# Optimization experiments

Measured on AMD Instinct MI355X. Metric: run time of the kernel, lower is better.

## Reference

```python
import jax, jax.numpy as jnp
import numpy as np

EPS = 1e-9
KERNEL = 3


def kernel_tile(x, kernel, stride):
    """im2col-style patch extraction. x: [B,H,W,...] -> [B,OH,OW,kernel*kernel,depth]."""
    B, H, W = x.shape[:3]
    depth = int(np.prod(x.shape[3:]))
    x = x.reshape(B, H, W, depth)
    OH = (H - kernel) // stride + 1
    OW = (W - kernel) // stride + 1
    patches = jnp.stack(
        [x[:, i:i + (OH - 1) * stride + 1:stride, j:j + (OW - 1) * stride + 1:stride, :]
         for i in range(kernel) for j in range(kernel)], axis=3)
    return patches  # [B,OH,OW,k*k,depth]


def em_routing(votes, i_act, beta_v, beta_a, routings):
    # votes: [B,S,S,I,O,16], i_act: [B,S,S,I], beta_*: [1,1,1,O]
    I, O = votes.shape[-3], votes.shape[-2]
    rr = jnp.full((I, O, 1), 1.0 / O, dtype=votes.dtype)
    i_act = i_act[..., None, None]           # [B,S,S,I,1,1]
    bv = beta_v[..., None, :, None]          # [1,1,1,1,O,1]
    ba = beta_a[..., None, :, None]
    it_min, it_max = 1.0, min(float(routings), 3.0)
    o_mean = o_act = None
    for it in range(routings):
        inv_temp = it_min + (it_max - it_min) * it / max(1.0, routings - 1.0)
        # M-step
        rr_prime = rr * i_act                                        # [B,S,S,I,O,1]
        rr_sum = jnp.sum(rr_prime, axis=-3, keepdims=True)           # [B,S,S,1,O,1]
        o_mean = jnp.sum(rr_prime * votes, axis=-3, keepdims=True) / rr_sum  # [B,S,S,1,O,16]
        o_stdv = jnp.sqrt(jnp.sum(rr_prime * jnp.square(votes - o_mean), axis=-3, keepdims=True) / rr_sum)
        o_cost = (bv + jnp.log(o_stdv + EPS)) * rr_sum               # [B,S,S,1,O,16]
        o_act = jax.nn.sigmoid(inv_temp * (ba - jnp.sum(o_cost, axis=-1, keepdims=True)))  # [B,S,S,1,O,1]
        if it < routings - 1:
            # E-step: log Gaussian prob of each vote under each output capsule
            o_p = (-jnp.sum(jnp.square(votes - o_mean) / (2.0 * jnp.square(o_stdv)), axis=-1, keepdims=True)
                   - jnp.sum(jnp.log(o_stdv + EPS), axis=-1, keepdims=True))  # [B,S,S,I,O,1]
            zz = jnp.log(o_act + EPS) + o_p
            rr = jax.nn.softmax(zz, axis=-2)                          # softmax over O
    pose = jnp.squeeze(o_mean, axis=-3)      # [B,S,S,O,16]
    act = jnp.squeeze(o_act, axis=(-3, -1))  # [B,S,S,O]
    return pose, act


def setup_inputs() -> dict:
    key = jax.random.key(0)
    ks = jax.random.split(key, 5)
    B, H, W, I_SIZE, O_SIZE = 4, 14, 14, 32, 32
    inputs_pose = jax.random.normal(ks[0], (B, H, W, I_SIZE, 4, 4), dtype=jnp.float32)
    inputs_activation = jax.random.uniform(ks[1], (B, H, W, I_SIZE), dtype=jnp.float32)
    w = jax.random.normal(ks[2], (1, 3 * 3 * I_SIZE, O_SIZE, 4, 4), dtype=jnp.float32)
    beta_v = 0.1 * jax.random.normal(ks[3], (1, 1, 1, O_SIZE), dtype=jnp.float32)
    beta_a = 0.1 * jax.random.normal(ks[4], (1, 1, 1, O_SIZE), dtype=jnp.float32)
    return {"inputs_pose": inputs_pose, "inputs_activation": inputs_activation,
            "w": w, "beta_v": beta_v, "beta_a": beta_a, "stride": 1, "routings": 3}


def reference(inputs_pose, inputs_activation, w, beta_v, beta_a, stride, routings):
    B = inputs_pose.shape[0]
    pose_size = inputs_pose.shape[-1]            # 4
    i_size = inputs_pose.shape[3]
    o_size = w.shape[2]
    tp = kernel_tile(inputs_pose, KERNEL, stride)        # [B,S,S,9,i*16]
    ta = kernel_tile(inputs_activation, KERNEL, stride)  # [B,S,S,9,i]
    S = ta.shape[1]
    I = KERNEL * KERNEL * i_size
    poses = tp.reshape(-1, I, pose_size, pose_size)      # [N,I,4,4], N = B*S*S
    acts = ta.reshape(B, S, S, I)
    # vote transform: per (input capsule, output capsule) 4x4 matmul
    votes = jnp.einsum('nipq,ioqr->niopr', poses, w[0])  # [N,I,O,4,4]
    votes = votes.reshape(B, S, S, I, o_size, pose_size * pose_size)
    pose, activation = em_routing(votes, acts, beta_v, beta_a, routings)
    pose = pose.reshape(B, S, S, o_size, pose_size, pose_size)
    return pose, activation
```

## Files before the change

kernel.cpp:

```cpp
#include <hip/hip_runtime.h>
#include <math.h>

namespace {

constexpr int SOUT = 12;
constexpr int OCAP = 32;
constexpr int PD   = 16;
constexpr int NI   = 288;
constexpr int SUBS = 4;
constexpr int ISUB = NI / SUBS;
constexpr int NPOS = 4 * SOUT * SOUT;
constexpr float EPSF = 1e-9f;
constexpr int CHUNK = 33 * 32;
constexpr size_t POSE_OUT = (size_t)NPOS * OCAP * PD;

typedef float v2f __attribute__((ext_vector_type(2)));

__device__ __forceinline__ v2f vfma(v2f a, v2f b, v2f c) { return __builtin_elementwise_fma(a, b, c); }
__device__ __forceinline__ v2f splat(float a) { v2f r; r.x = a; r.y = a; return r; }

template<int CTRL>
__device__ __forceinline__ float dppf(float x) {
    return __int_as_float(__builtin_amdgcn_update_dpp(0, __float_as_int(x), CTRL, 0xF, 0xF, true));
}
#define SWZ16(x) __int_as_float(__builtin_amdgcn_ds_swizzle(__float_as_int(x), (16 << 10) | 0x1F))

__device__ __forceinline__ float redsum32(float x) {
    x += dppf<0xB1>(x);
    x += dppf<0x4E>(x);
    x += dppf<0x141>(x);
    x += dppf<0x140>(x);
    x += SWZ16(x);
    return x;
}

__device__ __forceinline__ void loadW(const float* __restrict__ p, v2f (&W)[8]) {
    const float4 w0 = *reinterpret_cast<const float4*>(p);
    const float4 w1 = *reinterpret_cast<const float4*>(p + 4);
    const float4 w2 = *reinterpret_cast<const float4*>(p + 8);
    const float4 w3 = *reinterpret_cast<const float4*>(p + 12);
    W[0].x=w0.x; W[0].y=w0.y; W[1].x=w0.z; W[1].y=w0.w;
    W[2].x=w1.x; W[2].y=w1.y; W[3].x=w1.z; W[3].y=w1.w;
    W[4].x=w2.x; W[4].y=w2.y; W[5].x=w2.z; W[5].y=w2.w;
    W[6].x=w3.x; W[6].y=w3.y; W[7].x=w3.z; W[7].y=w3.w;
}

__device__ __forceinline__ void vote8(const float* __restrict__ pr, const v2f (&W)[8], v2f (&v)[8]) {
    #pragma unroll
    for (int p = 0; p < 4; ++p) {
        const float4 pv = *reinterpret_cast<const float4*>(pr + p * 4);
        #pragma unroll
        for (int h = 0; h < 2; ++h) {
            v2f acc = splat(pv.w) * W[6 + h];
            acc = vfma(splat(pv.z), W[4 + h], acc);
            acc = vfma(splat(pv.y), W[2 + h], acc);
            acc = vfma(splat(pv.x), W[0 + h], acc);
            v[p * 2 + h] = acc;
        }
    }
}

__device__ __forceinline__ constexpr int DH(int h) { return (h >> 1) * 4 + (h & 1) * 2; }

template<int SWEEP>
__global__ __launch_bounds__(256, 2)
void sweep_kernel(const float* __restrict__ pose_in,
                  const float* __restrict__ act_in,
                  const float* __restrict__ wmat,
                  const float* __restrict__ beta_v,
                  const float* __restrict__ beta_a,
                  const float* __restrict__ prev,
                  float* __restrict__ outbuf)
{
    __shared__ __align__(16) float sP[ISUB * PD];
    __shared__ float sA[ISUB];
    __shared__ __align__(8) float sStat[OCAP][2 * PD + 2];
    __shared__ float sBias[OCAP];
    __shared__ float sRed[2][33][33];

    const int bid = blockIdx.x;
    const int n   = bid >> 2;
    const int sub = bid & 3;
    const int b   = n / (SOUT * SOUT);
    const int yx  = n % (SOUT * SOUT);
    const int y   = yx / SOUT;
    const int x   = yx % SOUT;

    const int t    = threadIdx.x;
    const int wave = t >> 6;
    const int o    = t & 31;
    const int slot = t >> 5;
    const int half = slot & 1;

    {
        const float4* src = reinterpret_cast<const float4*>(pose_in);
        float4* dst = reinterpret_cast<float4*>(sP);
        for (int u = t; u < ISUB * 4; u += 256) {
            const int il = u >> 2;
            const int i  = sub * ISUB + il;
            const int k = i >> 5, c = i & 31;
            const int ki = k / 3, kj = k - ki * 3;
            const int cell = (b * 14 + y + ki) * 14 + (x + kj);
            dst[u] = src[(size_t)(cell * 32 + c) * 4 + (u & 3)];
        }
        if (t < ISUB) {
            const int i = sub * ISUB + t;
            const int k = i >> 5, c = i & 31;
            const int ki = k / 3, kj = k - ki * 3;
            const int cell = (b * 14 + y + ki) * 14 + (x + kj);
            sA[t] = act_in[(size_t)cell * 32 + c];
        }
    }

    if constexpr (SWEEP > 0) {
        const int oo = t >> 3, dp = t & 7, d0 = dp * 2;
        const float* base = prev + (size_t)n * (SUBS * CHUNK);
        float s0 = 0.f, S1a = 0.f, S1b = 0.f, S2a = 0.f, S2b = 0.f;
        #pragma unroll
        for (int s = 0; s < SUBS; ++s) {
            const float* c = base + s * CHUNK;
            s0  += c[32 * 32 + oo];
            S1a += c[(d0)      * 32 + oo];
            S1b += c[(d0 + 1)  * 32 + oo];
            S2a += c[(16 + d0) * 32 + oo];
            S2b += c[(17 + d0) * 32 + oo];
        }
        const float inv = 1.f / s0;
        const float m0 = S1a * inv, m1 = S1b * inv;
        const float v0 = fmaxf(fmaf(-m0, m0, S2a * inv), 0.f);
        const float v1 = fmaxf(fmaf(-m1, m1, S2b * inv), 0.f);
        const float i20 = 0.5f / fmaxf(v0, 1e-30f);
        const float i21 = 0.5f / fmaxf(v1, 1e-30f);
        float ll = __logf(sqrtf(v0) + EPSF) + __logf(sqrtf(v1) + EPSF);
        float c0 = m0 * m0 * i20 + m1 * m1 * i21;
        sStat[oo][d0]          = i20;
        sStat[oo][d0 + 1]      = i21;
        sStat[oo][16 + d0]     = -2.f * m0 * i20;
        sStat[oo][17 + d0]     = -2.f * m1 * i21;
        #pragma unroll
        for (int m = 1; m <= 4; m <<= 1) {
            ll += __shfl_xor(ll, m, 8);
            c0 += __shfl_xor(c0, m, 8);
        }
        if (dp == 0) {
            const float cost = s0 * fmaf(16.f, beta_v[oo], ll);
            const float oact = 1.f / (1.f + __expf(-(float)SWEEP * (beta_a[oo] - cost)));
            sBias[oo] = __logf(oact + EPSF) - ll - c0;
        }
    }
    __syncthreads();

    float bias_r = 0.f;
    v2f i2r[8], ngr[8];
    if constexpr (SWEEP > 0) {
        bias_r = sBias[o];
        #pragma unroll
        for (int h = 0; h < 8; ++h) {
            i2r[h] = *reinterpret_cast<const v2f*>(&sStat[o][2 * h]);
            ngr[h] = *reinterpret_cast<const v2f*>(&sStat[o][16 + 2 * h]);
        }
    }

    v2f s1[8], s2[8];
    float s0acc = 0.f;
    #pragma unroll
    for (int h = 0; h < 8; ++h) { s1[h] = splat(0.f); s2[h] = splat(0.f); }

    const float* wbase = wmat + ((size_t)(sub * ISUB + slot) * OCAP + o) * PD;

    v2f WA[8], WB[8];
    loadW(wbase, WA);

#define STEP(st, Wc, Wn)                                                   \
    {                                                                      \
        if ((st) < 8) loadW(wbase + (size_t)((st) + 1) * 4096, Wn);        \
        const int il = (st) * 8 + slot;                                    \
        v2f v[8];                                                          \
        vote8(&sP[il * PD], Wc, v);                                        \
        const float a_i = sA[il];                                          \
        float rrp;                                                         \
        if constexpr (SWEEP == 0) {                                        \
            rrp = a_i * (1.0f / 32.0f);                                    \
        } else {                                                           \
            v2f ts2 = splat(0.f);                                          \
            _Pragma("unroll")                                              \
            for (int h = 0; h < 8; ++h) {                                  \
                const v2f tmp = vfma(v[h], i2r[h], ngr[h]);                \
                ts2 = vfma(v[h], tmp, ts2);                                \
            }                                                              \
             \
            const float zz = bias_r - (ts2.x + ts2.y);                     \
            const float e = __expf(zz);                                    \
            const float es = redsum32(e);                                  \
            rrp = __fdividef(e, es) * a_i;                                 \
        }                                                                  \
        s0acc += rrp;                                                      \
        const v2f rr2 = splat(rrp);                                        \
        _Pragma("unroll")                                                  \
        for (int h = 0; h < 8; ++h) {                                      \
            const v2f rv = rr2 * v[h];                                     \
            s1[h] = s1[h] + rv;                                            \
            s2[h] = vfma(rv, v[h], s2[h]);                                 \
        }                                                                  \
    }

    STEP(0, WA, WB); STEP(1, WB, WA); STEP(2, WA, WB); STEP(3, WB, WA);
    STEP(4, WA, WB); STEP(5, WB, WA); STEP(6, WA, WB); STEP(7, WB, WA);
    STEP(8, WA, WB);
#undef STEP

    #pragma unroll
    for (int h = 0; h < 8; ++h) {
        s1[h].x += __shfl_xor(s1[h].x, 32, 64);
        s1[h].y += __shfl_xor(s1[h].y, 32, 64);
        s2[h].x += __shfl_xor(s2[h].x, 32, 64);
        s2[h].y += __shfl_xor(s2[h].y, 32, 64);
    }
    s0acc += __shfl_xor(s0acc, 32, 64);

    if (wave < 2 && half == 0) {
        #pragma unroll
        for (int h = 0; h < 8; ++h) {
            sRed[wave][DH(h)][o]          = s1[h].x;
            sRed[wave][DH(h) + 1][o]      = s1[h].y;
            sRed[wave][16 + DH(h)][o]     = s2[h].x;
            sRed[wave][16 + DH(h) + 1][o] = s2[h].y;
        }
        sRed[wave][32][o] = s0acc;
    }
    __syncthreads();
    if (wave >= 2 && half == 0) {
        #pragma unroll
        for (int h = 0; h < 8; ++h) {
            sRed[wave - 2][DH(h)][o]          += s1[h].x;
            sRed[wave - 2][DH(h) + 1][o]      += s1[h].y;
            sRed[wave - 2][16 + DH(h)][o]     += s2[h].x;
            sRed[wave - 2][16 + DH(h) + 1][o] += s2[h].y;
        }
        sRed[wave - 2][32][o] += s0acc;
    }
    __syncthreads();

    float* dstc = outbuf + (size_t)bid * CHUNK;
    const int oc = t & 31;
    for (int j = t >> 5; j < 33; j += 8)
        dstc[j * 32 + oc] = sRed[0][j][oc] + sRed[1][j][oc];
}

__global__ __launch_bounds__(256, 4)
void final_kernel(const float* __restrict__ prev,
                  const float* __restrict__ beta_v,
                  const float* __restrict__ beta_a,
                  float* __restrict__ out)
{
    const int n  = blockIdx.x;
    const int t  = threadIdx.x;
    const int oo = t >> 3, dp = t & 7, d0 = dp * 2;
    const float* base = prev + (size_t)n * (SUBS * CHUNK);
    float s0 = 0.f, S1a = 0.f, S1b = 0.f, S2a = 0.f, S2b = 0.f;
    #pragma unroll
    for (int s = 0; s < SUBS; ++s) {
        const float* c = base + s * CHUNK;
        s0  += c[32 * 32 + oo];
        S1a += c[(d0)      * 32 + oo];
        S1b += c[(d0 + 1)  * 32 + oo];
        S2a += c[(16 + d0) * 32 + oo];
        S2b += c[(17 + d0) * 32 + oo];
    }
    const float inv = 1.f / s0;
    const float m0 = S1a * inv, m1 = S1b * inv;
    out[(size_t)n * (OCAP * PD) + oo * PD + d0]     = m0;
    out[(size_t)n * (OCAP * PD) + oo * PD + d0 + 1] = m1;

    const float v0 = fmaxf(fmaf(-m0, m0, S2a * inv), 0.f);
    const float v1 = fmaxf(fmaf(-m1, m1, S2b * inv), 0.f);
    float lt = __logf(sqrtf(v0) + EPSF) + __logf(sqrtf(v1) + EPSF);
    lt += __shfl_xor(lt, 1, 8);
    lt += __shfl_xor(lt, 2, 8);
    lt += __shfl_xor(lt, 4, 8);
    if (dp == 0) {
        const float cost = s0 * fmaf(16.f, beta_v[oo], lt);
        const float oact = 1.f / (1.f + __expf(-3.0f * (beta_a[oo] - cost)));
        out[POSE_OUT + (size_t)n * OCAP + oo] = oact;
    }
}

}

extern "C" void kernel_launch(void* const* d_in, const int* in_sizes, int n_in,
                              void* d_out, int out_size, void* d_ws, size_t ws_size,
                              hipStream_t stream) {
    const float* pose_in = (const float*)d_in[0];
    const float* act_in  = (const float*)d_in[1];
    const float* wmat    = (const float*)d_in[2];
    const float* beta_v  = (const float*)d_in[3];
    const float* beta_a  = (const float*)d_in[4];
    float* out = (float*)d_out;

    float* bufA = (float*)d_ws;
    float* bufB = bufA + (size_t)NPOS * SUBS * CHUNK;

    dim3 block(256);
    dim3 gridS(NPOS);
    dim3 gridSweep(NPOS * SUBS);
    dim3 gridF(NPOS);

    sweep_kernel<0><<<gridSweep, block, 0, stream>>>(pose_in, act_in, wmat, beta_v, beta_a, nullptr, bufA);
    sweep_kernel<1><<<gridSweep, block, 0, stream>>>(pose_in, act_in, wmat, beta_v, beta_a, bufA, bufB);
    sweep_kernel<2><<<gridSweep, block, 0, stream>>>(pose_in, act_in, wmat, beta_v, beta_a, bufB, bufA);
    final_kernel<<<gridF, block, 0, stream>>>(bufA, beta_v, beta_a, out);
}
```

Before: 116.0 us.

## Fuse all EM routing sweeps and final step into one kernel per position

Result: faster. 106.8 us (-7.9%).

```diff
diff --git a/kernel.cpp b/kernel.cpp
--- a/kernel.cpp
+++ b/kernel.cpp
@@ -7,11 +7,8 @@
 constexpr int OCAP = 32;
 constexpr int PD   = 16;
 constexpr int NI   = 288;
-constexpr int SUBS = 4;
-constexpr int ISUB = NI / SUBS;
 constexpr int NPOS = 4 * SOUT * SOUT;
 constexpr float EPSF = 1e-9f;
-constexpr int CHUNK = 33 * 32;
 constexpr size_t POSE_OUT = (size_t)NPOS * OCAP * PD;
 
 typedef float v2f __attribute__((ext_vector_type(2)));
@@ -60,31 +57,25 @@
     }
 }
 
-__device__ __forceinline__ constexpr int DH(int h) { return (h >> 1) * 4 + (h & 1) * 2; }
-
-template<int SWEEP>
 __global__ __launch_bounds__(256, 2)
-void sweep_kernel(const float* __restrict__ pose_in,
-                  const float* __restrict__ act_in,
-                  const float* __restrict__ wmat,
-                  const float* __restrict__ beta_v,
-                  const float* __restrict__ beta_a,
-                  const float* __restrict__ prev,
-                  float* __restrict__ outbuf)
+void caps_fused(const float* __restrict__ pose_in,
+                const float* __restrict__ act_in,
+                const float* __restrict__ wmat,
+                const float* __restrict__ beta_v,
+                const float* __restrict__ beta_a,
+                float* __restrict__ out)
 {
-    __shared__ __align__(16) float sP[ISUB * PD];
-    __shared__ float sA[ISUB];
+    __shared__ __align__(16) float sP[NI * PD];
+    __shared__ float sA[NI];
     __shared__ __align__(8) float sStat[OCAP][2 * PD + 2];
     __shared__ float sBias[OCAP];
     __shared__ float sRed[2][33][33];
 
-    const int bid = blockIdx.x;
-    const int n   = bid >> 2;
-    const int sub = bid & 3;
-    const int b   = n / (SOUT * SOUT);
-    const int yx  = n % (SOUT * SOUT);
-    const int y   = yx / SOUT;
-    const int x   = yx % SOUT;
+    const int n  = blockIdx.x;
+    const int b  = n / (SOUT * SOUT);
+    const int yx = n % (SOUT * SOUT);
+    const int y  = yx / SOUT;
+    const int x  = yx % SOUT;
 
     const int t    = threadIdx.x;
     const int wave = t >> 6;
@@ -95,193 +86,163 @@
     {
         const float4* src = reinterpret_cast<const float4*>(pose_in);
         float4* dst = reinterpret_cast<float4*>(sP);
-        for (int u = t; u < ISUB * 4; u += 256) {
-            const int il = u >> 2;
-            const int i  = sub * ISUB + il;
+        for (int u = t; u < NI * 4; u += 256) {
+            const int i = u >> 2, comp = u & 3;
             const int k = i >> 5, c = i & 31;
             const int ki = k / 3, kj = k - ki * 3;
             const int cell = (b * 14 + y + ki) * 14 + (x + kj);
-            dst[u] = src[(size_t)(cell * 32 + c) * 4 + (u & 3)];
-        }
-        if (t < ISUB) {
-            const int i = sub * ISUB + t;
-            const int k = i >> 5, c = i & 31;
+            dst[u] = src[(size_t)(cell * 32 + c) * 4 + comp];
+        }
+        for (int u = t; u < NI; u += 256) {
+            const int k = u >> 5, c = u & 31;
             const int ki = k / 3, kj = k - ki * 3;
             const int cell = (b * 14 + y + ki) * 14 + (x + kj);
-            sA[t] = act_in[(size_t)cell * 32 + c];
-        }
-    }
-
-    if constexpr (SWEEP > 0) {
-        const int oo = t >> 3, dp = t & 7, d0 = dp * 2;
-        const float* base = prev + (size_t)n * (SUBS * CHUNK);
-        float s0 = 0.f, S1a = 0.f, S1b = 0.f, S2a = 0.f, S2b = 0.f;
-        #pragma unroll
-        for (int s = 0; s < SUBS; ++s) {
-            const float* c = base + s * CHUNK;
-            s0  += c[32 * 32 + oo];
-            S1a += c[(d0)      * 32 + oo];
-            S1b += c[(d0 + 1)  * 32 + oo];
-            S2a += c[(16 + d0) * 32 + oo];
-            S2b += c[(17 + d0) * 32 + oo];
-        }
-        const float inv = 1.f / s0;
-        const float m0 = S1a * inv, m1 = S1b * inv;
-        const float v0 = fmaxf(fmaf(-m0, m0, S2a * inv), 0.f);
-        const float v1 = fmaxf(fmaf(-m1, m1, S2b * inv), 0.f);
-        const float i20 = 0.5f / fmaxf(v0, 1e-30f);
-        const float i21 = 0.5f / fmaxf(v1, 1e-30f);
-        float ll = __logf(sqrtf(v0) + EPSF) + __logf(sqrtf(v1) + EPSF);
-        float c0 = m0 * m0 * i20 + m1 * m1 * i21;
-        sStat[oo][d0]          = i20;
-        sStat[oo][d0 + 1]      = i21;
-        sStat[oo][16 + d0]     = -2.f * m0 * i20;
-        sStat[oo][17 + d0]     = -2.f * m1 * i21;
-        #pragma unroll
-        for (int m = 1; m <= 4; m <<= 1) {
-            ll += __shfl_xor(ll, m, 8);
-            c0 += __shfl_xor(c0, m, 8);
-        }
-        if (dp == 0) {
-            const float cost = s0 * fmaf(16.f, beta_v[oo], ll);
-            const float oact = 1.f / (1.f + __expf(-(float)SWEEP * (beta_a[oo] - cost)));
-            sBias[oo] = __logf(oact + EPSF) - ll - c0;
+            sA[u] = act_in[(size_t)cell * 32 + c];
         }
     }
     __syncthreads();
 
-    float bias_r = 0.f;
-    v2f i2r[8], ngr[8];
-    if constexpr (SWEEP > 0) {
-        bias_r = sBias[o];
+    const float* wth = wmat + ((size_t)(slot * OCAP + o)) * PD;
+
+    #pragma unroll 1
+    for (int sweep = 0; sweep < 3; ++sweep) {
+        float bias_r = 0.f;
+        v2f i2r[8], ngr[8];
+        if (sweep > 0) {
+            bias_r = sBias[o];
+            #pragma unroll
+            for (int h = 0; h < 8; ++h) {
+                i2r[h] = *reinterpret_cast<const v2f*>(&sStat[o][2 * h]);
+                ngr[h] = *reinterpret_cast<const v2f*>(&sStat[o][16 + 2 * h]);
+            }
+        }
+
+        v2f s1[8], s2[8];
+        float s0acc = 0.f;
+        #pragma unroll
+        for (int h = 0; h < 8; ++h) { s1[h] = splat(0.f); s2[h] = splat(0.f); }
+
+        v2f WA[8], WB[8];
+        loadW(wth, WA);
+
+#define STEP(st_, Wc, Wn)                                                  \
+        {                                                                  \
+            if ((st_) < 35) loadW(wth + (size_t)((st_) + 1) * 4096, Wn);   \
+            const int il = (st_) * 8 + slot;                               \
+            v2f v[8];                                                      \
+            vote8(&sP[il * PD], Wc, v);                                    \
+            const float a_i = sA[il];                                      \
+            float rrp;                                                     \
+            if (sweep == 0) {                                              \
+                rrp = a_i * (1.0f / 32.0f);                                \
+            } else {                                                       \
+                v2f ts2 = splat(0.f);                                      \
+                _Pragma("unroll")                                          \
+                for (int h = 0; h < 8; ++h) {                              \
+                    const v2f tmp = vfma(v[h], i2r[h], ngr[h]);            \
+                    ts2 = vfma(v[h], tmp, ts2);                            \
+                }                                                          \
+                  \
+                const float zz = bias_r - (ts2.x + ts2.y);                 \
+                const float e = __expf(zz);                                \
+                const float es = redsum32(e);                              \
+                rrp = __fdividef(e, es) * a_i;                             \
+            }                                                              \
+            s0acc += rrp;                                                  \
+            const v2f rr2 = splat(rrp);                                    \
+            _Pragma("unroll")                                              \
+            for (int h = 0; h < 8; ++h) {                                  \
+                const v2f rv = rr2 * v[h];                                 \
+                s1[h] = s1[h] + rv;                                        \
+                s2[h] = vfma(rv, v[h], s2[h]);                             \
+            }                                                              \
+        }
+
+        #pragma unroll 1
+        for (int kk = 0; kk < 18; ++kk) {
+            STEP(2 * kk,     WA, WB);
+            STEP(2 * kk + 1, WB, WA);
+        }
+#undef STEP
+
         #pragma unroll
         for (int h = 0; h < 8; ++h) {
-            i2r[h] = *reinterpret_cast<const v2f*>(&sStat[o][2 * h]);
-            ngr[h] = *reinterpret_cast<const v2f*>(&sStat[o][16 + 2 * h]);
-        }
-    }
-
-    v2f s1[8], s2[8];
-    float s0acc = 0.f;
-    #pragma unroll
-    for (int h = 0; h < 8; ++h) { s1[h] = splat(0.f); s2[h] = splat(0.f); }
-
-    const float* wbase = wmat + ((size_t)(sub * ISUB + slot) * OCAP + o) * PD;
-
-    v2f WA[8], WB[8];
-    loadW(wbase, WA);
-
-#define STEP(st, Wc, Wn)                                                   \
-    {                                                                      \
-        if ((st) < 8) loadW(wbase + (size_t)((st) + 1) * 4096, Wn);        \
-        const int il = (st) * 8 + slot;                                    \
-        v2f v[8];                                                          \
-        vote8(&sP[il * PD], Wc, v);                                        \
-        const float a_i = sA[il];                                          \
-        float rrp;                                                         \
-        if constexpr (SWEEP == 0) {                                        \
-            rrp = a_i * (1.0f / 32.0f);                                    \
-        } else {                                                           \
-            v2f ts2 = splat(0.f);                                          \
-            _Pragma("unroll")                                              \
-            for (int h = 0; h < 8; ++h) {                                  \
-                const v2f tmp = vfma(v[h], i2r[h], ngr[h]);                \
-                ts2 = vfma(v[h], tmp, ts2);                                \
-            }                                                              \
-             \
-            const float zz = bias_r - (ts2.x + ts2.y);                     \
-            const float e = __expf(zz);                                    \
-            const float es = redsum32(e);                                  \
-            rrp = __fdividef(e, es) * a_i;                                 \
-        }                                                                  \
-        s0acc += rrp;                                                      \
-        const v2f rr2 = splat(rrp);                                        \
-        _Pragma("unroll")                                                  \
-        for (int h = 0; h < 8; ++h) {                                      \
-            const v2f rv = rr2 * v[h];                                     \
-            s1[h] = s1[h] + rv;                                            \
-            s2[h] = vfma(rv, v[h], s2[h]);                                 \
-        }                                                                  \
-    }
-
-    STEP(0, WA, WB); STEP(1, WB, WA); STEP(2, WA, WB); STEP(3, WB, WA);
-    STEP(4, WA, WB); STEP(5, WB, WA); STEP(6, WA, WB); STEP(7, WB, WA);
-    STEP(8, WA, WB);
-#undef STEP
-
-    #pragma unroll
-    for (int h = 0; h < 8; ++h) {
-        s1[h].x += __shfl_xor(s1[h].x, 32, 64);
-        s1[h].y += __shfl_xor(s1[h].y, 32, 64);
-        s2[h].x += __shfl_xor(s2[h].x, 32, 64);
-        s2[h].y += __shfl_xor(s2[h].y, 32, 64);
-    }
-    s0acc += __shfl_xor(s0acc, 32, 64);
-
-    if (wave < 2 && half == 0) {
-        #pragma unroll
-        for (int h = 0; h < 8; ++h) {
-            sRed[wave][DH(h)][o]          = s1[h].x;
-            sRed[wave][DH(h) + 1][o]      = s1[h].y;
-            sRed[wave][16 + DH(h)][o]     = s2[h].x;
-            sRed[wave][16 + DH(h) + 1][o] = s2[h].y;
-        }
-        sRed[wave][32][o] = s0acc;
-    }
-    __syncthreads();
-    if (wave >= 2 && half == 0) {
-        #pragma unroll
-        for (int h = 0; h < 8; ++h) {
-            sRed[wave - 2][DH(h)][o]          += s1[h].x;
-            sRed[wave - 2][DH(h) + 1][o]      += s1[h].y;
-            sRed[wave - 2][16 + DH(h)][o]     += s2[h].x;
-            sRed[wave - 2][16 + DH(h) + 1][o] += s2[h].y;
-        }
-        sRed[wave - 2][32][o] += s0acc;
-    }
-    __syncthreads();
-
-    float* dstc = outbuf + (size_t)bid * CHUNK;
-    const int oc = t & 31;
-    for (int j = t >> 5; j < 33; j += 8)
-        dstc[j * 32 + oc] = sRed[0][j][oc] + sRed[1][j][oc];
-}
-
-__global__ __launch_bounds__(256, 4)
-void final_kernel(const float* __restrict__ prev,
-                  const float* __restrict__ beta_v,
-                  const float* __restrict__ beta_a,
-                  float* __restrict__ out)
-{
-    const int n  = blockIdx.x;
-    const int t  = threadIdx.x;
-    const int oo = t >> 3, dp = t & 7, d0 = dp * 2;
-    const float* base = prev + (size_t)n * (SUBS * CHUNK);
-    float s0 = 0.f, S1a = 0.f, S1b = 0.f, S2a = 0.f, S2b = 0.f;
-    #pragma unroll
-    for (int s = 0; s < SUBS; ++s) {
-        const float* c = base + s * CHUNK;
-        s0  += c[32 * 32 + oo];
-        S1a += c[(d0)      * 32 + oo];
-        S1b += c[(d0 + 1)  * 32 + oo];
-        S2a += c[(16 + d0) * 32 + oo];
-        S2b += c[(17 + d0) * 32 + oo];
-    }
-    const float inv = 1.f / s0;
-    const float m0 = S1a * inv, m1 = S1b * inv;
-    out[(size_t)n * (OCAP * PD) + oo * PD + d0]     = m0;
-    out[(size_t)n * (OCAP * PD) + oo * PD + d0 + 1] = m1;
-
-    const float v0 = fmaxf(fmaf(-m0, m0, S2a * inv), 0.f);
-    const float v1 = fmaxf(fmaf(-m1, m1, S2b * inv), 0.f);
-    float lt = __logf(sqrtf(v0) + EPSF) + __logf(sqrtf(v1) + EPSF);
-    lt += __shfl_xor(lt, 1, 8);
-    lt += __shfl_xor(lt, 2, 8);
-    lt += __shfl_xor(lt, 4, 8);
-    if (dp == 0) {
-        const float cost = s0 * fmaf(16.f, beta_v[oo], lt);
-        const float oact = 1.f / (1.f + __expf(-3.0f * (beta_a[oo] - cost)));
-        out[POSE_OUT + (size_t)n * OCAP + oo] = oact;
+            s1[h].x += __shfl_xor(s1[h].x, 32, 64);
+            s1[h].y += __shfl_xor(s1[h].y, 32, 64);
+            s2[h].x += __shfl_xor(s2[h].x, 32, 64);
+            s2[h].y += __shfl_xor(s2[h].y, 32, 64);
+        }
+        s0acc += __shfl_xor(s0acc, 32, 64);
+
+        if (wave < 2 && half == 0) {
+            #pragma unroll
+            for (int h = 0; h < 8; ++h) {
+                sRed[wave][2 * h][o]          = s1[h].x;
+                sRed[wave][2 * h + 1][o]      = s1[h].y;
+                sRed[wave][16 + 2 * h][o]     = s2[h].x;
+                sRed[wave][16 + 2 * h + 1][o] = s2[h].y;
+            }
+            sRed[wave][32][o] = s0acc;
+        }
+        __syncthreads();
+        if (wave >= 2 && half == 0) {
+            #pragma unroll
+            for (int h = 0; h < 8; ++h) {
+                sRed[wave - 2][2 * h][o]          += s1[h].x;
+                sRed[wave - 2][2 * h + 1][o]      += s1[h].y;
+                sRed[wave - 2][16 + 2 * h][o]     += s2[h].x;
+                sRed[wave - 2][16 + 2 * h + 1][o] += s2[h].y;
+            }
+            sRed[wave - 2][32][o] += s0acc;
+        }
+        __syncthreads();
+
+        {
+            const int oo = t >> 3, dp = t & 7, d0 = dp * 2;
+            const float S0  = sRed[0][32][oo]      + sRed[1][32][oo];
+            const float S1a = sRed[0][d0][oo]      + sRed[1][d0][oo];
+            const float S1b = sRed[0][d0 + 1][oo]  + sRed[1][d0 + 1][oo];
+            const float S2a = sRed[0][16 + d0][oo] + sRed[1][16 + d0][oo];
+            const float S2b = sRed[0][17 + d0][oo] + sRed[1][17 + d0][oo];
+            const float inv = 1.f / S0;
+            const float m0 = S1a * inv, m1 = S1b * inv;
+            const float v0 = fmaxf(fmaf(-m0, m0, S2a * inv), 0.f);
+            const float v1 = fmaxf(fmaf(-m1, m1, S2b * inv), 0.f);
+            float ll = __logf(sqrtf(v0) + EPSF) + __logf(sqrtf(v1) + EPSF);
+
+            if (sweep < 2) {
+                const float i20 = 0.5f / fmaxf(v0, 1e-30f);
+                const float i21 = 0.5f / fmaxf(v1, 1e-30f);
+                float c0 = m0 * m0 * i20 + m1 * m1 * i21;
+                sStat[oo][d0]      = i20;
+                sStat[oo][d0 + 1]  = i21;
+                sStat[oo][16 + d0] = -2.f * m0 * i20;
+                sStat[oo][17 + d0] = -2.f * m1 * i21;
+                #pragma unroll
+                for (int m = 1; m <= 4; m <<= 1) {
+                    ll += __shfl_xor(ll, m, 8);
+                    c0 += __shfl_xor(c0, m, 8);
+                }
+                if (dp == 0) {
+                    const float cost = S0 * fmaf(16.f, beta_v[oo], ll);
+                    const float invtemp = 1.0f + (float)sweep;
+                    const float oact = 1.f / (1.f + __expf(-invtemp * (beta_a[oo] - cost)));
+                    sBias[oo] = __logf(oact + EPSF) - ll - c0;
+                }
+            } else {
+                float2 pv; pv.x = m0; pv.y = m1;
+                *reinterpret_cast<float2*>(out + (size_t)n * (OCAP * PD) + oo * PD + d0) = pv;
+                #pragma unroll
+                for (int m = 1; m <= 4; m <<= 1)
+                    ll += __shfl_xor(ll, m, 8);
+                if (dp == 0) {
+                    const float cost = S0 * fmaf(16.f, beta_v[oo], ll);
+                    const float oact = 1.f / (1.f + __expf(-3.0f * (beta_a[oo] - cost)));
+                    out[POSE_OUT + (size_t)n * OCAP + oo] = oact;
+                }
+            }
+        }
+        __syncthreads();
     }
 }
 
@@ -297,16 +258,6 @@
     const float* beta_a  = (const float*)d_in[4];
     float* out = (float*)d_out;
 
-    float* bufA = (float*)d_ws;
-    float* bufB = bufA + (size_t)NPOS * SUBS * CHUNK;
-
-    dim3 block(256);
-    dim3 gridS(NPOS);
-    dim3 gridSweep(NPOS * SUBS);
-    dim3 gridF(NPOS);
-
-    sweep_kernel<0><<<gridSweep, block, 0, stream>>>(pose_in, act_in, wmat, beta_v, beta_a, nullptr, bufA);
-    sweep_kernel<1><<<gridSweep, block, 0, stream>>>(pose_in, act_in, wmat, beta_v, beta_a, bufA, bufB);
-    sweep_kernel<2><<<gridSweep, block, 0, stream>>>(pose_in, act_in, wmat, beta_v, beta_a, bufB, bufA);
-    final_kernel<<<gridF, block, 0, stream>>>(bufA, beta_v, beta_a, out);
-}
+    caps_fused<<<dim3(NPOS), dim3(256), 0, stream>>>(
+        pose_in, act_in, wmat, beta_v, beta_a, out);
+}
```
